# Kernel optimization log

Measured on AMD Instinct MI355X. Metric: run time of the kernel, lower is better.

The kernel has to match this reference:

```python
import jax, jax.numpy as jnp
import numpy as np

B, C, H, D, HID = 1024, 64, 64, 256, 256

def setup_inputs() -> dict:
    key = jax.random.key(0)
    k1, k2, k3, k4, k5, k6, k7, k8 = jax.random.split(key, 8)
    candidate_news_vector = jax.random.normal(k1, (B, C, D), dtype=jnp.float32)
    clicked_news_vector = jax.random.normal(k2, (B, H, D), dtype=jnp.float32)
    mask_cand = jax.random.randint(k3, (B, C), 0, 2).astype(bool).at[:, 0].set(True)
    mask_hist = jax.random.randint(k4, (B, H), 0, 2).astype(bool).at[:, 0].set(True)
    # nn.Linear default init: U(-1/sqrt(fan_in), 1/sqrt(fan_in))
    s1 = 1.0 / np.sqrt(2 * D)
    s2 = 1.0 / np.sqrt(HID)
    W1 = jax.random.uniform(k5, (HID, 2 * D), minval=-s1, maxval=s1, dtype=jnp.float32)
    b1 = jax.random.uniform(k6, (HID,), minval=-s1, maxval=s1, dtype=jnp.float32)
    W2 = jax.random.uniform(k7, (1, HID), minval=-s2, maxval=s2, dtype=jnp.float32)
    b2 = jax.random.uniform(k8, (1,), minval=-s2, maxval=s2, dtype=jnp.float32)
    return {"candidate_news_vector": candidate_news_vector,
            "clicked_news_vector": clicked_news_vector,
            "mask_cand": mask_cand, "mask_hist": mask_hist,
            "W1": W1, "b1": b1, "W2": W2, "b2": b2}

def reference(candidate_news_vector, clicked_news_vector, mask_cand, mask_hist, W1, b1, W2, b2):
    d = candidate_news_vector.shape[-1]
    w2 = W2[0]                                  # [HID]
    # Two stacked Linears with no nonlinearity collapse exactly:
    # score = (W2 @ W1_c) . cand + (W2 @ W1_h) . hist + (W2 @ b1 + b2)
    v_c = W1[:, :d].T @ w2                      # [D]
    v_h = W1[:, d:].T @ w2                      # [D]
    bias = jnp.dot(w2, b1) + b2[0]
    scores = (jnp.einsum('bcd,d->bc', candidate_news_vector, v_c)[:, :, None]
              + jnp.einsum('bhd,d->bh', clicked_news_vector, v_h)[:, None, :]
              + bias)                           # [B, C, H]
    neg = jnp.finfo(scores.dtype).min
    scores = jnp.where(mask_hist[:, None, :], scores, neg)
    weights = jax.nn.softmax(scores, axis=-1)   # [B, C, H]
    weights = jnp.where(mask_cand[:, :, None], weights, 0.0)
    user_vector = jnp.einsum('bch,bhd->bcd', weights, clicked_news_vector)
    return user_vector
```

## Files before the change

kernel.cpp:

```cpp
#include <hip/hip_runtime.h>
#include <math.h>

#define NB 1024
#define NC 64
#define NH 64
#define ND 256
#define NHID 256

typedef float f4 __attribute__((ext_vector_type(4)));

#define WS_PART_OFF 1024

__device__ __forceinline__ bool read_mask(const void* m, int idx, int mode) {
  if (mode == 2) return ((const float*)m)[idx] != 0.0f;
  if (mode == 1) return ((const unsigned char*)m)[idx] != 0;
  return ((const int*)m)[idx] != 0;
}

__device__ __forceinline__ void detect_mode(const unsigned int* mask_cand,
                                            const unsigned int* mask_hist,
                                            int* dst) {
  int sawf = 0; unsigned int big = 0;
  for (int i = 0; i < 32; ++i) {
    unsigned int a = mask_hist[i], b = mask_cand[i];
    if (a == 0x3f800000u || b == 0x3f800000u) sawf = 1;
    if ((a > 1u && a != 0x3f800000u) || (b > 1u && b != 0x3f800000u)) big = 1;
  }
  *dst = sawf ? 2 : (big ? 1 : 0);
}

__device__ __forceinline__ float dot4(f4 a, f4 b) {
  return fmaf(a.x, b.x, fmaf(a.y, b.y, fmaf(a.z, b.z, a.w * b.w)));
}

#define BFLY(p) { p += __shfl_xor(p, 32); p += __shfl_xor(p, 16); p += __shfl_xor(p, 8); \
                  p += __shfl_xor(p, 4);  p += __shfl_xor(p, 2);  p += __shfl_xor(p, 1); }

__global__ __launch_bounds__(256) void precompute_p1(
    const float* __restrict__ W1, const float* __restrict__ W2,
    float* __restrict__ ws)
{
  const int g = blockIdx.x;
  const int d = threadIdx.x;
  float acc = 0.f;
  #pragma unroll
  for (int jj = 0; jj < 4; ++jj) {
    int j = g * 4 + jj;
    acc = fmaf(W1[(size_t)j * (2 * ND) + ND + d], W2[j], acc);
  }
  ws[WS_PART_OFF + g * ND + d] = acc;
}

__global__ __launch_bounds__(256) void precompute_p2(
    const unsigned int* __restrict__ mask_cand,
    const unsigned int* __restrict__ mask_hist,
    float* __restrict__ ws)
{
  const int d = threadIdx.x;
  float acc = 0.f;
  #pragma unroll 8
  for (int g = 0; g < 64; ++g) acc += ws[WS_PART_OFF + g * ND + d];
  ws[d] = acc;
  if (d == 0) detect_mode(mask_cand, mask_hist, (int*)ws + ND);
}

__global__ __launch_bounds__(1024) void precompute_fallback(
    const float* __restrict__ W1, const float* __restrict__ W2,
    const unsigned int* __restrict__ mask_cand,
    const unsigned int* __restrict__ mask_hist,
    float* __restrict__ ws)
{
  __shared__ float w2_lds[NHID];
  __shared__ float partial[4][ND];
  int t = threadIdx.x;
  if (t < NHID) w2_lds[t] = W2[t];
  __syncthreads();
  int d = t & (ND - 1);
  int g = t >> 8;
  float acc = 0.f;
  #pragma unroll 8
  for (int j = g * 64; j < g * 64 + 64; ++j)
    acc = fmaf(W1[(size_t)j * (2 * ND) + ND + d], w2_lds[j], acc);
  partial[g][d] = acc;
  __syncthreads();
  if (t < ND)
    ws[t] = partial[0][t] + partial[1][t] + partial[2][t] + partial[3][t];
  if (t == 0) detect_mode(mask_cand, mask_hist, (int*)ws + ND);
}

#define LOADB(R0,R1,R2,R3,R4,R5,R6,R7, H0)                                     \
  R0 = hp4[((H0) + 0) * 64 + lane]; R1 = hp4[((H0) + 1) * 64 + lane];          \
  R2 = hp4[((H0) + 2) * 64 + lane]; R3 = hp4[((H0) + 3) * 64 + lane];          \
  R4 = hp4[((H0) + 4) * 64 + lane]; R5 = hp4[((H0) + 5) * 64 + lane];          \
  R6 = hp4[((H0) + 6) * 64 + lane]; R7 = hp4[((H0) + 7) * 64 + lane];

#define PROCB(R0,R1,R2,R3,R4,R5,R6,R7, H0)                                     \
  {                                                                            \
    float p0 = dot4(R0, vhq), p1 = dot4(R1, vhq), p2 = dot4(R2, vhq),          \
          p3 = dot4(R3, vhq), p4 = dot4(R4, vhq), p5 = dot4(R5, vhq),          \
          p6 = dot4(R6, vhq), p7 = dot4(R7, vhq);                              \
    BFLY(p0) BFLY(p1) BFLY(p2) BFLY(p3) BFLY(p4) BFLY(p5) BFLY(p6) BFLY(p7)    \
    p0 = ((mh >> ((H0) + 0)) & 1) ? p0 : -3.0e38f;                             \
    p1 = ((mh >> ((H0) + 1)) & 1) ? p1 : -3.0e38f;                             \
    p2 = ((mh >> ((H0) + 2)) & 1) ? p2 : -3.0e38f;                             \
    p3 = ((mh >> ((H0) + 3)) & 1) ? p3 : -3.0e38f;                             \
    p4 = ((mh >> ((H0) + 4)) & 1) ? p4 : -3.0e38f;                             \
    p5 = ((mh >> ((H0) + 5)) & 1) ? p5 : -3.0e38f;                             \
    p6 = ((mh >> ((H0) + 6)) & 1) ? p6 : -3.0e38f;                             \
    p7 = ((mh >> ((H0) + 7)) & 1) ? p7 : -3.0e38f;                             \
    float pm = fmaxf(fmaxf(fmaxf(p0, p1), fmaxf(p2, p3)),                      \
                     fmaxf(fmaxf(p4, p5), fmaxf(p6, p7)));                     \
    float mn = fmaxf(mrun, pm);                                                \
    float sc = expf(mrun - mn);                                                \
    float e0 = expf(p0 - mn), e1 = expf(p1 - mn), e2 = expf(p2 - mn),          \
          e3 = expf(p3 - mn), e4 = expf(p4 - mn), e5 = expf(p5 - mn),          \
          e6 = expf(p6 - mn), e7 = expf(p7 - mn);                              \
    srun = srun * sc + ((e0 + e1) + (e2 + e3)) + ((e4 + e5) + (e6 + e7));      \
    acc = acc * sc;                                                            \
    acc += e0 * R0; acc += e1 * R1; acc += e2 * R2; acc += e3 * R3;            \
    acc += e4 * R4; acc += e5 * R5; acc += e6 * R6; acc += e7 * R7;            \
    mrun = mn;                                                                 \
  }

__global__ __launch_bounds__(256) void flash_kernel(
    const float* __restrict__ hist,
    const void* __restrict__ mask_cand_v,
    const void* __restrict__ mask_hist_v,
    const float* __restrict__ ws,
    float* __restrict__ out)
{
  const int t = threadIdx.x, lane = t & 63, w = t >> 6;
  const int b = blockIdx.x * 4 + w;

  const int mode = ((const int*)ws)[ND];
  const f4* hp4 = reinterpret_cast<const f4*>(hist) + (size_t)b * 4096;
  const f4 vhq = reinterpret_cast<const f4*>(ws)[lane];

  const unsigned long long mh =
      __ballot(read_mask(mask_hist_v, b * NH + lane, mode));
  const unsigned long long mc =
      __ballot(read_mask(mask_cand_v, b * NC + lane, mode));

  float mrun = -3.0e38f, srun = 0.f;
  f4 acc = {0.f, 0.f, 0.f, 0.f};
  f4 x0, x1, x2, x3, x4, x5, x6, x7;
  f4 y0, y1, y2, y3, y4, y5, y6, y7;

  LOADB(x0,x1,x2,x3,x4,x5,x6,x7, 0)
  LOADB(y0,y1,y2,y3,y4,y5,y6,y7, 8)
  PROCB(x0,x1,x2,x3,x4,x5,x6,x7, 0)
  LOADB(x0,x1,x2,x3,x4,x5,x6,x7, 16)
  PROCB(y0,y1,y2,y3,y4,y5,y6,y7, 8)
  LOADB(y0,y1,y2,y3,y4,y5,y6,y7, 24)
  PROCB(x0,x1,x2,x3,x4,x5,x6,x7, 16)
  LOADB(x0,x1,x2,x3,x4,x5,x6,x7, 32)
  PROCB(y0,y1,y2,y3,y4,y5,y6,y7, 24)
  LOADB(y0,y1,y2,y3,y4,y5,y6,y7, 40)
  PROCB(x0,x1,x2,x3,x4,x5,x6,x7, 32)
  LOADB(x0,x1,x2,x3,x4,x5,x6,x7, 48)
  PROCB(y0,y1,y2,y3,y4,y5,y6,y7, 40)
  LOADB(y0,y1,y2,y3,y4,y5,y6,y7, 56)
  PROCB(x0,x1,x2,x3,x4,x5,x6,x7, 48)
  PROCB(y0,y1,y2,y3,y4,y5,y6,y7, 56)

  const f4 uv = acc * (1.0f / srun);
  const f4 zero = {0.f, 0.f, 0.f, 0.f};
  f4* ob4 = reinterpret_cast<f4*>(out) + (size_t)b * 4096;
  #pragma unroll
  for (int c = 0; c < 64; ++c)
    ob4[c * 64 + lane] = ((mc >> c) & 1ull) ? uv : zero;
}

extern "C" void kernel_launch(void* const* d_in, const int* in_sizes, int n_in,
                              void* d_out, int out_size, void* d_ws, size_t ws_size,
                              hipStream_t stream) {
  (void)in_sizes; (void)n_in; (void)out_size;
  const float* hist = (const float*)d_in[1];
  const void*  mask_cand = d_in[2];
  const void*  mask_hist = d_in[3];
  const float* W1 = (const float*)d_in[4];
  const float* W2 = (const float*)d_in[6];
  float* ws = (float*)d_ws;
  float* out = (float*)d_out;

  if (ws_size >= (size_t)(WS_PART_OFF + 64 * ND) * sizeof(float)) {
    precompute_p1<<<64, 256, 0, stream>>>(W1, W2, ws);
    precompute_p2<<<1, 256, 0, stream>>>(
        (const unsigned int*)mask_cand, (const unsigned int*)mask_hist, ws);
  } else {
    precompute_fallback<<<1, 1024, 0, stream>>>(
        W1, W2, (const unsigned int*)mask_cand, (const unsigned int*)mask_hist, ws);
  }
  flash_kernel<<<NB / 4, 256, 0, stream>>>(hist, mask_cand, mask_hist, ws, out);
}
```

Before: 40.00 us.

## Split flash attention and output broadcast into separate kernels with deeper prefetch

The fused kernel is split in two. The first computes the per-batch user vector with a four-deep register prefetch of history rows and writes it to workspace. The second is a wide kernel (4096 blocks) that broadcasts that vector to the masked candidate rows using nontemporal stores. The aim is to spread the 64 MB output write across many more waves than the 256-block fused kernel could. The cost is an extra launch, a workspace round trip, and fewer waves per CU in the attention kernel because of the higher register use.

New measurement: 48.17 us. +20.4%, slower.

```diff
diff --git a/kernel.cpp b/kernel.cpp
--- a/kernel.cpp
+++ b/kernel.cpp
@@ -10,6 +10,7 @@
 typedef float f4 __attribute__((ext_vector_type(4)));
 
 #define WS_PART_OFF 1024
+#define WS_UV_OFF   32768
 
 __device__ __forceinline__ bool read_mask(const void* m, int idx, int mode) {
   if (mode == 2) return ((const float*)m)[idx] != 0.0f;
@@ -122,14 +123,80 @@
     mrun = mn;                                                                 \
   }
 
-__global__ __launch_bounds__(256) void flash_kernel(
+__global__ __launch_bounds__(256, 1) void score_uv_flash(
+    const float* __restrict__ hist,
+    const void* __restrict__ mask_hist_v,
+    const float* __restrict__ ws,
+    float* __restrict__ uv_out)
+{
+  const int tid = threadIdx.x, lane = tid & 63, w = tid >> 6;
+  const int b = blockIdx.x * 4 + w;
+
+  const int mode = ((const int*)ws)[ND];
+  const f4* hp4 = reinterpret_cast<const f4*>(hist) + (size_t)b * 4096;
+  const f4 vhq = reinterpret_cast<const f4*>(ws)[lane];
+
+  const unsigned long long mh =
+      __ballot(read_mask(mask_hist_v, b * NH + lane, mode));
+
+  float mrun = -3.0e38f, srun = 0.f;
+  f4 acc = {0.f, 0.f, 0.f, 0.f};
+  f4 x0, x1, x2, x3, x4, x5, x6, x7;
+  f4 y0, y1, y2, y3, y4, y5, y6, y7;
+  f4 z0, z1, z2, z3, z4, z5, z6, z7;
+  f4 u0, u1, u2, u3, u4, u5, u6, u7;
+
+  LOADB(x0,x1,x2,x3,x4,x5,x6,x7, 0)
+  LOADB(y0,y1,y2,y3,y4,y5,y6,y7, 8)
+  LOADB(z0,z1,z2,z3,z4,z5,z6,z7, 16)
+  LOADB(u0,u1,u2,u3,u4,u5,u6,u7, 24)
+  PROCB(x0,x1,x2,x3,x4,x5,x6,x7, 0)
+  LOADB(x0,x1,x2,x3,x4,x5,x6,x7, 32)
+  PROCB(y0,y1,y2,y3,y4,y5,y6,y7, 8)
+  LOADB(y0,y1,y2,y3,y4,y5,y6,y7, 40)
+  PROCB(z0,z1,z2,z3,z4,z5,z6,z7, 16)
+  LOADB(z0,z1,z2,z3,z4,z5,z6,z7, 48)
+  PROCB(u0,u1,u2,u3,u4,u5,u6,u7, 24)
+  LOADB(u0,u1,u2,u3,u4,u5,u6,u7, 56)
+  PROCB(x0,x1,x2,x3,x4,x5,x6,x7, 32)
+  PROCB(y0,y1,y2,y3,y4,y5,y6,y7, 40)
+  PROCB(z0,z1,z2,z3,z4,z5,z6,z7, 48)
+  PROCB(u0,u1,u2,u3,u4,u5,u6,u7, 56)
+
+  const f4 uv = acc * (1.0f / srun);
+  reinterpret_cast<f4*>(uv_out)[b * 64 + lane] = uv;
+}
+
+__global__ __launch_bounds__(256) void broadcast_kernel(
+    const float* __restrict__ uv_src,
+    const void* __restrict__ mask_cand_v,
+    const float* __restrict__ ws,
+    float* __restrict__ out)
+{
+  const int bid = blockIdx.x;
+  const int b = bid >> 2, q = bid & 3;
+  const int t = threadIdx.x, lane = t & 63, g = t >> 6;
+  const int mode = ((const int*)ws)[ND];
+  const f4 uv = reinterpret_cast<const f4*>(uv_src)[b * 64 + lane];
+  f4* ob4 = reinterpret_cast<f4*>(out) + (size_t)b * 4096;
+  const f4 zero = {0.f, 0.f, 0.f, 0.f};
+  #pragma unroll
+  for (int j = 0; j < 4; ++j) {
+    int c = q * 16 + g * 4 + j;
+    bool mc = read_mask(mask_cand_v, b * NC + c, mode);
+    f4 val = mc ? uv : zero;
+    __builtin_nontemporal_store(val, &ob4[c * 64 + lane]);
+  }
+}
+
+__global__ __launch_bounds__(256) void flash_fallback_kernel(
     const float* __restrict__ hist,
     const void* __restrict__ mask_cand_v,
     const void* __restrict__ mask_hist_v,
     const float* __restrict__ ws,
     float* __restrict__ out)
 {
-  const int t = threadIdx.x, lane = t & 63, w = t >> 6;
+  const int tid = threadIdx.x, lane = tid & 63, w = tid >> 6;
   const int b = blockIdx.x * 4 + w;
 
   const int mode = ((const int*)ws)[ND];
@@ -183,7 +250,10 @@
   float* ws = (float*)d_ws;
   float* out = (float*)d_out;
 
-  if (ws_size >= (size_t)(WS_PART_OFF + 64 * ND) * sizeof(float)) {
+  const bool mid = ws_size >= (size_t)(WS_PART_OFF + 64 * ND) * sizeof(float);
+  const bool big = ws_size >= (size_t)(WS_UV_OFF + NB * ND) * sizeof(float);
+
+  if (mid) {
     precompute_p1<<<64, 256, 0, stream>>>(W1, W2, ws);
     precompute_p2<<<1, 256, 0, stream>>>(
         (const unsigned int*)mask_cand, (const unsigned int*)mask_hist, ws);
@@ -191,5 +261,11 @@
     precompute_fallback<<<1, 1024, 0, stream>>>(
         W1, W2, (const unsigned int*)mask_cand, (const unsigned int*)mask_hist, ws);
   }
-  flash_kernel<<<NB / 4, 256, 0, stream>>>(hist, mask_cand, mask_hist, ws, out);
-}
+
+  if (big) {
+    score_uv_flash<<<NB / 4, 256, 0, stream>>>(hist, mask_hist, ws, ws + WS_UV_OFF);
+    broadcast_kernel<<<NB * 4, 256, 0, stream>>>(ws + WS_UV_OFF, mask_cand, ws, out);
+  } else {
+    flash_fallback_kernel<<<NB / 4, 256, 0, stream>>>(hist, mask_cand, mask_hist, ws, out);
+  }
+}
```
